# Kernel tuning notes

Hardware: AMD Instinct MI355X
Metric: run time of the kernel (lower is better)

Reference implementation:

```python
import jax, jax.numpy as jnp
import numpy as np

N = 8192          # total genes
B = 16            # number of ragged batch groups (equal-size here: 512 each)
D = 768           # hidden_dim
NEG = -1.0e9      # mask fill value used by the original module


def setup_inputs() -> dict:
    key = jax.random.key(0)
    ks = jax.random.split(key, 10)
    s = 0.02
    inp = {
        "gene_embeddings": jax.random.normal(ks[0], (N, D), dtype=jnp.float32),
        # sorted group ids: 16 contiguous groups of 512 genes
        "batch": (jnp.arange(N) // (N // B)).astype(jnp.int64),
        "Wq": jax.random.normal(ks[1], (D, D), dtype=jnp.float32) * s,
        "bq": jnp.zeros((D,), dtype=jnp.float32),
        "Wk": jax.random.normal(ks[2], (D, D), dtype=jnp.float32) * s,
        "bk": jnp.zeros((D,), dtype=jnp.float32),
        "Wv": jax.random.normal(ks[3], (D, D), dtype=jnp.float32) * s,
        "bv": jnp.zeros((D,), dtype=jnp.float32),
        "Wo": jax.random.normal(ks[4], (D, D), dtype=jnp.float32) * s,
        "bo": jnp.zeros((D,), dtype=jnp.float32),
        "beta": jnp.ones((1,), dtype=jnp.float32) * 0.1,
    }
    return inp


def reference(gene_embeddings, batch, Wq, bq, Wk, bk, Wv, bv, Wo, bo, beta):
    # Single-head attention over full hidden_dim (num_heads unused in original).
    x = gene_embeddings
    q = x @ Wq.T + bq                      # [N, D]
    k = x @ Wk.T + bk
    v = x @ Wv.T + bv
    scale = 1.0 / jnp.sqrt(jnp.asarray(D, dtype=x.dtype))
    scores = (q @ k.T) * scale             # [N, N]
    # block-diagonal group mask + diagonal self-mask (same -1e9 fill as torch code)
    same_group = batch[:, None] == batch[None, :]
    eye = jnp.eye(N, dtype=bool)
    allow = same_group & (~eye)
    scores = jnp.where(allow, scores, NEG)
    weights = jax.nn.softmax(scores, axis=-1)   # dropout in eval mode -> identity
    dyn = weights @ v                       # [N, D]
    dyn = dyn @ Wo.T + bo
    return x + beta * dyn
```

## Files before the change

kernel.cpp:

```cpp
#include <hip/hip_runtime.h>
#include <hip/hip_bf16.h>
#include <cstdint>

using u16 = unsigned short;
using u32 = unsigned int;

typedef __bf16 bf16x8 __attribute__((ext_vector_type(8)));
typedef float  f32x4  __attribute__((ext_vector_type(4)));

__device__ __forceinline__ u32 f2b2(float a, float b) {
    __hip_bfloat162 h = __float22bfloat162_rn(float2{a, b});
    u32 u;
    __builtin_memcpy(&u, &h, 4);
    return u;
}
__device__ __forceinline__ float b2f(u16 b) {
    u32 u = (u32)b << 16;
    float f;
    __builtin_memcpy(&f, &u, 4);
    return f;
}

__device__ __forceinline__ void gload_lds16(const u16* g, u16* l) {
    __builtin_amdgcn_global_load_lds(
        (const __attribute__((address_space(1))) void*)g,
        (__attribute__((address_space(3))) void*)l,
        16, 0, 0);
}

__launch_bounds__(256)
__global__ void pack_kernel(const float* __restrict__ x,
                            const float* __restrict__ Wq,
                            const float* __restrict__ Wk,
                            const float* __restrict__ Wv,
                            const float* __restrict__ Wo,
                            const float* __restrict__ bq,
                            const float* __restrict__ bv,
                            const float* __restrict__ bo,
                            u16* __restrict__ xb,
                            u16* __restrict__ Wob,
                            u16* __restrict__ WqT,
                            u16* __restrict__ WkT,
                            u16* __restrict__ WvT,
                            float* __restrict__ czk,
                            float* __restrict__ bvoo)
{
    __shared__ u16 tl[64][72];
    const int b = blockIdx.x, tid = threadIdx.x;

    if (b < 3360) {
        int c = b * 256 + tid;
        long e = (long)c * 8;
        const float* src; u16* dst; long off;
        if (e < 6291456L) { src = x;  dst = xb;  off = e; }
        else              { src = Wo; dst = Wob; off = e - 6291456L; }
        float4 v0 = *(const float4*)(src + off);
        float4 v1 = *(const float4*)(src + off + 4);
        uint4 o;
        o.x = f2b2(v0.x, v0.y); o.y = f2b2(v0.z, v0.w);
        o.z = f2b2(v1.x, v1.y); o.w = f2b2(v1.z, v1.w);
        *(uint4*)(dst + off) = o;
    } else if (b < 3792) {
        int t = b - 3360;
        int w = t / 144, tt = t % 144;
        int tr = tt / 12, tc = tt % 12;
        const float* src0 = (w == 0) ? Wq : (w == 1) ? Wk : Wv;
        u16* dst0 = (w == 0) ? WqT : (w == 1) ? WkT : WvT;
        int lr = tid >> 2, lcb = (tid & 3) * 16;
        const float* src = src0 + (long)(tr * 64 + lr) * 768 + tc * 64 + lcb;
#pragma unroll
        for (int q = 0; q < 4; q++) {
            float4 v = *(const float4*)(src + q * 4);
            u32 p0 = f2b2(v.x, v.y), p1 = f2b2(v.z, v.w);
            tl[lr][lcb + q * 4 + 0] = (u16)p0;
            tl[lr][lcb + q * 4 + 1] = (u16)(p0 >> 16);
            tl[lr][lcb + q * 4 + 2] = (u16)p1;
            tl[lr][lcb + q * 4 + 3] = (u16)(p1 >> 16);
        }
        __syncthreads();
        int li = tid >> 2, lkb = (tid & 3) * 16;
        u16 o[16];
#pragma unroll
        for (int j = 0; j < 16; j++) o[j] = tl[lkb + j][li];
        u16* dst = dst0 + (long)(tc * 64 + li) * 768 + tr * 64 + lkb;
#pragma unroll
        for (int j = 0; j < 16; j++) dst[j] = o[j];
    } else if (b < 3984) {
        int wave = tid >> 6, lane = tid & 63;
        int j = (b - 3792) * 4 + wave;
        float acc = 0.f;
#pragma unroll
        for (int i = 0; i < 12; i++) {
            int rr = i * 64 + lane;
            acc += Wk[(long)rr * 768 + j] * bq[rr];
        }
#pragma unroll
        for (int d = 32; d; d >>= 1) acc += __shfl_xor(acc, d);
        if (lane == 0) czk[j] = acc;
    } else {
        int wave = tid >> 6, lane = tid & 63;
        int j = (b - 3984) * 4 + wave;
        float acc = 0.f;
#pragma unroll
        for (int i = 0; i < 12; i++) {
            int k = i * 64 + lane;
            acc += Wo[(long)j * 768 + k] * bv[k];
        }
#pragma unroll
        for (int d = 32; d; d >>= 1) acc += __shfl_xor(acc, d);
        if (lane == 0) bvoo[j] = acc + bo[j];
    }
}

template<int TM, int TN, int MODE>
__device__ __forceinline__ void gemm_body(
        const u16* __restrict__ A, int lda, long sAz,
        const u16* __restrict__ B, int ldb, long sBz,
        void* __restrict__ Cv, int ldc, long sCz,
        int K,
        const float* __restrict__ bias,
        float scale,
        u16* __restrict__ vTout)
{
    constexpr int FI = TM / 32;
    constexpr int FJ = TN / 32;
    constexpr int CA = TM / 64;
    constexpr int CB = TN / 64;

    __shared__ u16 As[2][TM * 32];
    __shared__ u16 Bs[2][TN * 32];

    const int tid  = threadIdx.x;
    const int g    = blockIdx.z;
    const u16* Ab = A + (long)g * sAz + (long)blockIdx.y * TM * lda;
    const u16* Bb = B + (long)g * sBz + (long)blockIdx.x * TN * ldb;

    const int wave = tid >> 6, lane = tid & 63;
    const int wm = (wave >> 1) * (TM / 2), wn = (wave & 1) * (TN / 2);
    const int ln15 = lane & 15, lq = lane >> 4;

    f32x4 acc[FI][FJ];
#pragma unroll
    for (int i = 0; i < FI; i++)
#pragma unroll
        for (int j = 0; j < FJ; j++)
            acc[i][j] = (f32x4){0.f, 0.f, 0.f, 0.f};

    const int srow = lane >> 2;
    const int sc   = ((lane & 3) ^ ((lane >> 4) & 3)) * 8;
    const u16* Ag[CA]; const u16* Bg[CB];
    int Al[CA], Bl[CB];
#pragma unroll
    for (int t = 0; t < CA; t++) {
        int c = wave * CA + t;
        Ag[t] = Ab + (long)(c * 16 + srow) * lda + sc;
        Al[t] = c * 512;
    }
#pragma unroll
    for (int t = 0; t < CB; t++) {
        int c = wave * CB + t;
        Bg[t] = Bb + (long)(c * 16 + srow) * ldb + sc;
        Bl[t] = c * 512;
    }

    const int foff = ln15 * 32 + ((lq ^ (ln15 >> 2)) * 8);
    const int nk = K >> 5;

#pragma unroll
    for (int t = 0; t < CA; t++) gload_lds16(Ag[t], &As[0][Al[t]]);
#pragma unroll
    for (int t = 0; t < CB; t++) gload_lds16(Bg[t], &Bs[0][Bl[t]]);

    for (int kt = 0; kt < nk; kt++) {
        const int cur = kt & 1;
        __syncthreads();
        if (kt + 1 < nk) {
            const int k0 = (kt + 1) * 32, nxt = cur ^ 1;
#pragma unroll
            for (int t = 0; t < CA; t++) gload_lds16(Ag[t] + k0, &As[nxt][Al[t]]);
#pragma unroll
            for (int t = 0; t < CB; t++) gload_lds16(Bg[t] + k0, &Bs[nxt][Bl[t]]);
        }

        bf16x8 af[FI], bfr[FJ];
#pragma unroll
        for (int i = 0; i < FI; i++)
            af[i] = *(const bf16x8*)&As[cur][(wm / 16 + i) * 512 + foff];
#pragma unroll
        for (int j = 0; j < FJ; j++)
            bfr[j] = *(const bf16x8*)&Bs[cur][(wn / 16 + j) * 512 + foff];
#pragma unroll
        for (int i = 0; i < FI; i++)
#pragma unroll
            for (int j = 0; j < FJ; j++)
                acc[i][j] = __builtin_amdgcn_mfma_f32_16x16x32_bf16(af[i], bfr[j], acc[i][j], 0, 0, 0);
    }

    const int baseRow = blockIdx.y * TM + wm;
    const int baseCol = blockIdx.x * TN + wn;

    if constexpr (MODE == 0) {
        if (baseCol < 768) {
            u16* C = (u16*)Cv;
#pragma unroll
            for (int i = 0; i < FI; i++)
#pragma unroll
                for (int j = 0; j < FJ; j++) {
                    int col = baseCol + j * 16 + ln15;
                    float bb = bias[col];
                    u32 p01 = f2b2(acc[i][j][0] + bb, acc[i][j][1] + bb);
                    u32 p23 = f2b2(acc[i][j][2] + bb, acc[i][j][3] + bb);
                    long r0 = (long)(baseRow + i * 16 + lq * 4) * ldc + col;
                    C[r0]           = (u16)p01;
                    C[r0 + ldc]     = (u16)(p01 >> 16);
                    C[r0 + 2 * ldc] = (u16)p23;
                    C[r0 + 3 * ldc] = (u16)(p23 >> 16);
                }
        } else {
#pragma unroll
            for (int i = 0; i < FI; i++)
#pragma unroll
                for (int j = 0; j < FJ; j++) {
                    int col = baseCol + j * 16 + ln15;
                    uint2 o;
                    o.x = f2b2(acc[i][j][0], acc[i][j][1]);
                    o.y = f2b2(acc[i][j][2], acc[i][j][3]);
                    *(uint2*)(vTout + (long)(col - 768) * 8192
                              + baseRow + i * 16 + lq * 4) = o;
                }
        }
    } else {
        u16* C = (u16*)Cv + (long)g * sCz;
#pragma unroll
        for (int i = 0; i < FI; i++)
#pragma unroll
            for (int j = 0; j < FJ; j++) {
                int col = baseCol + j * 16 + ln15;
                u32 p01 = f2b2(acc[i][j][0], acc[i][j][1]);
                u32 p23 = f2b2(acc[i][j][2], acc[i][j][3]);
                long r0 = (long)(baseRow + i * 16 + lq * 4) * ldc + col;
                C[r0]           = (u16)p01;
                C[r0 + ldc]     = (u16)(p01 >> 16);
                C[r0 + 2 * ldc] = (u16)p23;
                C[r0 + 3 * ldc] = (u16)(p23 >> 16);
            }
    }
}

__launch_bounds__(256)
__global__ void k_ww(const u16* WA, const u16* WB, void* WZplus)
{
    gemm_body<64, 128, 3>(WA, 768, 589824L, WB, 768, 589824L,
                          WZplus, 768, -589824L, 768,
                          nullptr, 0.f, nullptr);
}
__launch_bounds__(256)
__global__ void k_zv(const u16* A, const u16* B, void* C, const float* bias,
                     u16* vTout)
{
    gemm_body<128, 128, 0>(A, 768, 0, B, 768, 0, C, 768, 0, 768,
                           bias, 0.f, vTout);
}

__launch_bounds__(512)
__global__ void k_fattn(const u16* __restrict__ zbuf,
                        const u16* __restrict__ xb,
                        const u16* __restrict__ vwT,
                        float* __restrict__ out,
                        const float* __restrict__ bvoo,
                        const float* __restrict__ betaPtr,
                        float scale)
{
    __shared__ __align__(16) u16 smem[57344];
    u16* zl = smem;
    u16* xB = smem + 24576;
    u16* Pl = smem;
    float* redM = (float*)(smem + 16384);
    float* redS = (float*)(smem + 16640);
    u16* Vs = smem + 18432;

    const int bx = blockIdx.x;
    const int lg = ((bx & 7) << 5) + (bx >> 3);
    const int g = lg >> 4, rt = lg & 15;

    const int tid = threadIdx.x;
    const int wave = tid >> 6, lane = tid & 63;
    const int ln15 = lane & 15, lq = lane >> 4;
    const int srow = lane >> 2;
    const int sc = ((lane & 3) ^ ((lane >> 4) & 3)) * 8;
    const int foff = ln15 * 32 + ((lq ^ (ln15 >> 2)) * 8);

    const long rowBase = (long)(g * 512 + rt * 32);
    const u16* Zb = zbuf + rowBase * 768;
    const u16* Xg = xb + (long)g * 512 * 768;

    const int wm = (wave >> 2) * 16;
    const int wn = (wave & 3) * 128;

#pragma unroll
    for (int n = 0; n < 6; n++) {
        int cc = n * 8 + wave;
        gload_lds16(Zb + (long)((cc & 1) * 16 + srow) * 768 + (cc >> 1) * 32 + sc,
                    &zl[cc * 512]);
    }
    const u16* Bg[4]; int Bl[4];
#pragma unroll
    for (int t = 0; t < 4; t++) {
        int c = wave * 4 + t;
        Bg[t] = Xg + (long)(c * 16 + srow) * 768 + sc;
        Bl[t] = c * 512;
    }
#pragma unroll
    for (int t = 0; t < 4; t++) gload_lds16(Bg[t], &xB[Bl[t]]);

    f32x4 acc[8];
#pragma unroll
    for (int j = 0; j < 8; j++) acc[j] = (f32x4){0.f, 0.f, 0.f, 0.f};

    for (int kt = 0; kt < 24; kt++) {
        const int cur = kt & 1;
        __syncthreads();
        if (kt + 1 < 24) {
            const int k0 = (kt + 1) * 32, nxt = cur ^ 1;
#pragma unroll
            for (int t = 0; t < 4; t++)
                gload_lds16(Bg[t] + k0, &xB[nxt * 16384 + Bl[t]]);
        }
        bf16x8 af = *(const bf16x8*)&zl[(kt * 2 + (wm >> 4)) * 512 + foff];
        bf16x8 bfr[8];
#pragma unroll
        for (int j = 0; j < 8; j++)
            bfr[j] = *(const bf16x8*)&xB[cur * 16384 + (wn / 16 + j) * 512 + foff];
#pragma unroll
        for (int j = 0; j < 8; j++)
            acc[j] = __builtin_amdgcn_mfma_f32_16x16x32_bf16(af, bfr[j], acc[j], 0, 0, 0);
    }

    __syncthreads();

#pragma unroll
    for (int sub = 0; sub < 4; sub++)
        gload_lds16(vwT + (long)(wave * 16 + srow) * 8192 + g * 512 + sub * 32 + sc,
                    &Vs[sub * 4096 + wave * 512]);

    float mx[4];
#pragma unroll
    for (int rr = 0; rr < 4; rr++) mx[rr] = -3.0e38f;
#pragma unroll
    for (int j = 0; j < 8; j++)
#pragma unroll
        for (int rr = 0; rr < 4; rr++) {
            const int col = wn + j * 16 + ln15;
            float v = acc[j][rr] * scale;
            if (rt * 32 + wm + lq * 4 + rr == col) v = -1.0e9f;
            acc[j][rr] = v;
            mx[rr] = fmaxf(mx[rr], v);
        }
#pragma unroll
    for (int rr = 0; rr < 4; rr++) {
        mx[rr] = fmaxf(mx[rr], __shfl_xor(mx[rr], 1));
        mx[rr] = fmaxf(mx[rr], __shfl_xor(mx[rr], 2));
        mx[rr] = fmaxf(mx[rr], __shfl_xor(mx[rr], 4));
        mx[rr] = fmaxf(mx[rr], __shfl_xor(mx[rr], 8));
    }
    if (ln15 == 0) {
#pragma unroll
        for (int rr = 0; rr < 4; rr++)
            redM[(wm + lq * 4 + rr) * 4 + (wave & 3)] = mx[rr];
    }
    __syncthreads();

    float m[4], s[4];
#pragma unroll
    for (int rr = 0; rr < 4; rr++) {
        float4 rm = *(const float4*)&redM[(wm + lq * 4 + rr) * 4];
        m[rr] = fmaxf(fmaxf(rm.x, rm.y), fmaxf(rm.z, rm.w));
        s[rr] = 0.f;
    }
#pragma unroll
    for (int j = 0; j < 8; j++)
#pragma unroll
        for (int rr = 0; rr < 4; rr++) {
            float p = __expf(acc[j][rr] - m[rr]);
            acc[j][rr] = p;
            s[rr] += p;
        }
#pragma unroll
    for (int rr = 0; rr < 4; rr++) {
        s[rr] += __shfl_xor(s[rr], 1);
        s[rr] += __shfl_xor(s[rr], 2);
        s[rr] += __shfl_xor(s[rr], 4);
        s[rr] += __shfl_xor(s[rr], 8);
    }
    if (ln15 == 0) {
#pragma unroll
        for (int rr = 0; rr < 4; rr++)
            redS[(wm + lq * 4 + rr) * 4 + (wave & 3)] = s[rr];
    }
#pragma unroll
    for (int j = 0; j < 8; j++) {
        const int col = wn + j * 16 + ln15;
        const int c8 = col >> 3, b7 = col & 7;
#pragma unroll
        for (int rr = 0; rr < 4; rr++) {
            const int row = wm + lq * 4 + rr;
            Pl[(row * 64 + (c8 ^ (row & 7))) * 8 + b7] = (u16)f2b2(acc[j][rr], acc[j][rr]);
        }
    }
    __syncthreads();

    float invS[4];
#pragma unroll
    for (int rr = 0; rr < 4; rr++) {
        float4 rs = *(const float4*)&redS[(wm + lq * 4 + rr) * 4];
        invS[rr] = 1.0f / (rs.x + rs.y + rs.z + rs.w);
    }

    const int prow = wm + ln15;
    bf16x8 apr[16];
#pragma unroll
    for (int k4 = 0; k4 < 16; k4++)
        apr[k4] = *(const bf16x8*)&Pl[(prow * 64 + ((k4 * 4 + lq) ^ (prow & 7))) * 8];

    const int wnP = (wave & 3) * 32;
    const float bet = betaPtr[0];
    f32x4 aP0 = (f32x4){0.f, 0.f, 0.f, 0.f};
    f32x4 aP1 = (f32x4){0.f, 0.f, 0.f, 0.f};

    for (int ct = 0; ct < 6; ct++) {
#pragma unroll
        for (int kn2 = 0; kn2 < 4; kn2++) {
            const int ts = ct * 4 + kn2;
            const int cur = ts & 1;
            __syncthreads();
            if (ts + 1 < 24) {
                const int tn = ts + 1, ctn = tn >> 2, kn = tn & 3;
                const int nxt = cur ^ 1;
#pragma unroll
                for (int sub = 0; sub < 4; sub++)
                    gload_lds16(vwT + (long)(ctn * 128 + wave * 16 + srow) * 8192
                                    + g * 512 + kn * 128 + sub * 32 + sc,
                                &Vs[nxt * 16384 + sub * 4096 + wave * 512]);
            }
#pragma unroll
            for (int sub = 0; sub < 4; sub++) {
                bf16x8 b0 = *(const bf16x8*)&Vs[cur * 16384 + sub * 4096
                                                + (wnP >> 4) * 512 + foff];
                bf16x8 b1 = *(const bf16x8*)&Vs[cur * 16384 + sub * 4096
                                                + ((wnP >> 4) + 1) * 512 + foff];
                aP0 = __builtin_amdgcn_mfma_f32_16x16x32_bf16(apr[kn2 * 4 + sub], b0, aP0, 0, 0, 0);
                aP1 = __builtin_amdgcn_mfma_f32_16x16x32_bf16(apr[kn2 * 4 + sub], b1, aP1, 0, 0, 0);
            }
        }
        {
            const u16* Xr = xb + (rowBase + wm + lq * 4) * 768;
            float* O = out + (rowBase + wm + lq * 4) * 768;
            {
                const int col = ct * 128 + wnP + ln15;
                const float bb = bvoo[col];
#pragma unroll
                for (int rr = 0; rr < 4; rr++)
                    O[rr * 768 + col] = b2f(Xr[rr * 768 + col])
                                        + bet * (invS[rr] * aP0[rr] + bb);
            }
            {
                const int col = ct * 128 + wnP + 16 + ln15;
                const float bb = bvoo[col];
#pragma unroll
                for (int rr = 0; rr < 4; rr++)
                    O[rr * 768 + col] = b2f(Xr[rr * 768 + col])
                                        + bet * (invS[rr] * aP1[rr] + bb);
            }
            aP0 = (f32x4){0.f, 0.f, 0.f, 0.f};
            aP1 = (f32x4){0.f, 0.f, 0.f, 0.f};
        }
    }
}

extern "C" void kernel_launch(void* const* d_in, const int* in_sizes, int n_in,
                              void* d_out, int out_size, void* d_ws, size_t ws_size,
                              hipStream_t stream)
{
    const float* x    = (const float*)d_in[0];
    const float* Wq   = (const float*)d_in[2];
    const float* bq   = (const float*)d_in[3];
    const float* Wk   = (const float*)d_in[4];
    const float* bk   = (const float*)d_in[5];
    const float* Wv   = (const float*)d_in[6];
    const float* bv   = (const float*)d_in[7];
    const float* Wo   = (const float*)d_in[8];
    const float* bo   = (const float*)d_in[9];
    const float* beta = (const float*)d_in[10];
    float* out = (float*)d_out;
    (void)bk;

    char* ws = (char*)d_ws;
    u16*   zbuf = (u16*)(ws + 0);
    u16*   vwT  = (u16*)(ws + 12582912);
    u16*   xb   = (u16*)(ws + 25165824);
    u16*   WA   = (u16*)(ws + 46137344);
    u16*   WB   = (u16*)(ws + 48496640);
    u16*   WZ   = (u16*)(ws + 50855936);
    float* czk  = (float*)(ws + 53215232);
    float* bvoo = (float*)(ws + 53218304);

    u16* Wob = WA;
    u16* WkT = WA + 589824;
    u16* WvT = WB;
    u16* WqT = WB + 589824;

    const float scale = 0.03608439182435161f;

    pack_kernel<<<4176, 256, 0, stream>>>(x, Wq, Wk, Wv, Wo, bq, bv, bo,
                                          xb, Wob, WqT, WkT, WvT, czk, bvoo);

    k_ww<<<dim3(6, 12, 2), 256, 0, stream>>>(WA, WB, (void*)(WZ + 589824L));

    k_zv<<<dim3(12, 64, 1), 256, 0, stream>>>(xb, WZ, (void*)zbuf, czk, vwT);

    k_fattn<<<dim3(256), 512, 0, stream>>>(zbuf, xb, vwT, out, bvoo, beta,
                                           scale);
}
```

Baseline: 193.9 us.

## Deepen LDS prefetch to two stages with explicit waitcnt and deferred epilogue

The QK^T and PV loops now issue global-to-LDS loads two tiles ahead instead of one. __syncthreads is replaced by explicit vmcnt/lgkmcnt waits and raw barriers, and s_setprio is raised around the MFMA bursts. In the PV stage, all six column-tile accumulators are kept in registers and the output epilogue is moved after the loop, so global loads and stores no longer sit between MFMA phases. The aim is to hide load latency and barrier stalls, at the cost of more registers, a second barrier per iteration, and hand-written wait counts that have to match the number of loads in flight.

```diff
diff --git a/kernel.cpp b/kernel.cpp
--- a/kernel.cpp
+++ b/kernel.cpp
@@ -27,6 +27,10 @@
         (__attribute__((address_space(3))) void*)l,
         16, 0, 0);
 }
+
+#define VMCNT(N)  asm volatile("s_waitcnt vmcnt(" #N ")" ::: "memory")
+#define LGKMCNT0  asm volatile("s_waitcnt lgkmcnt(0)" ::: "memory")
+#define BARRIER   asm volatile("s_barrier" ::: "memory")
 
 __launch_bounds__(256)
 __global__ void pack_kernel(const float* __restrict__ x,
@@ -312,6 +316,8 @@
     }
 #pragma unroll
     for (int t = 0; t < 4; t++) gload_lds16(Bg[t], &xB[Bl[t]]);
+#pragma unroll
+    for (int t = 0; t < 4; t++) gload_lds16(Bg[t] + 32, &xB[16384 + Bl[t]]);
 
     f32x4 acc[8];
 #pragma unroll
@@ -319,21 +325,27 @@
 
     for (int kt = 0; kt < 24; kt++) {
         const int cur = kt & 1;
-        __syncthreads();
-        if (kt + 1 < 24) {
-            const int k0 = (kt + 1) * 32, nxt = cur ^ 1;
-#pragma unroll
-            for (int t = 0; t < 4; t++)
-                gload_lds16(Bg[t] + k0, &xB[nxt * 16384 + Bl[t]]);
-        }
+        if (kt < 23) { VMCNT(4); } else { VMCNT(0); }
+        BARRIER;
         bf16x8 af = *(const bf16x8*)&zl[(kt * 2 + (wm >> 4)) * 512 + foff];
         bf16x8 bfr[8];
 #pragma unroll
         for (int j = 0; j < 8; j++)
             bfr[j] = *(const bf16x8*)&xB[cur * 16384 + (wn / 16 + j) * 512 + foff];
+        LGKMCNT0;
+        __builtin_amdgcn_sched_barrier(0);
+        BARRIER;
+        if (kt + 2 < 24) {
+            const int k0 = (kt + 2) * 32;
+#pragma unroll
+            for (int t = 0; t < 4; t++)
+                gload_lds16(Bg[t] + k0, &xB[cur * 16384 + Bl[t]]);
+        }
+        __builtin_amdgcn_s_setprio(1);
 #pragma unroll
         for (int j = 0; j < 8; j++)
             acc[j] = __builtin_amdgcn_mfma_f32_16x16x32_bf16(af, bfr[j], acc[j], 0, 0, 0);
+        __builtin_amdgcn_s_setprio(0);
     }
 
     __syncthreads();
@@ -342,6 +354,10 @@
     for (int sub = 0; sub < 4; sub++)
         gload_lds16(vwT + (long)(wave * 16 + srow) * 8192 + g * 512 + sub * 32 + sc,
                     &Vs[sub * 4096 + wave * 512]);
+#pragma unroll
+    for (int sub = 0; sub < 4; sub++)
+        gload_lds16(vwT + (long)(wave * 16 + srow) * 8192 + g * 512 + 128 + sub * 32 + sc,
+                    &Vs[16384 + sub * 4096 + wave * 512]);
 
     float mx[4];
 #pragma unroll
@@ -423,56 +439,63 @@
         apr[k4] = *(const bf16x8*)&Pl[(prow * 64 + ((k4 * 4 + lq) ^ (prow & 7))) * 8];
 
     const int wnP = (wave & 3) * 32;
-    const float bet = betaPtr[0];
-    f32x4 aP0 = (f32x4){0.f, 0.f, 0.f, 0.f};
-    f32x4 aP1 = (f32x4){0.f, 0.f, 0.f, 0.f};
-
+    f32x4 aP[6][2];
+#pragma unroll
+    for (int ct = 0; ct < 6; ct++) {
+        aP[ct][0] = (f32x4){0.f, 0.f, 0.f, 0.f};
+        aP[ct][1] = (f32x4){0.f, 0.f, 0.f, 0.f};
+    }
+
+#pragma unroll
     for (int ct = 0; ct < 6; ct++) {
 #pragma unroll
         for (int kn2 = 0; kn2 < 4; kn2++) {
             const int ts = ct * 4 + kn2;
             const int cur = ts & 1;
-            __syncthreads();
-            if (ts + 1 < 24) {
-                const int tn = ts + 1, ctn = tn >> 2, kn = tn & 3;
-                const int nxt = cur ^ 1;
+            if (ts < 23) { VMCNT(4); } else { VMCNT(0); }
+            BARRIER;
+            bf16x8 b0[4], b1[4];
+#pragma unroll
+            for (int sub = 0; sub < 4; sub++) {
+                b0[sub] = *(const bf16x8*)&Vs[cur * 16384 + sub * 4096
+                                              + (wnP >> 4) * 512 + foff];
+                b1[sub] = *(const bf16x8*)&Vs[cur * 16384 + sub * 4096
+                                              + ((wnP >> 4) + 1) * 512 + foff];
+            }
+            LGKMCNT0;
+            __builtin_amdgcn_sched_barrier(0);
+            BARRIER;
+            if (ts + 2 < 24) {
+                const int tn = ts + 2, ctn = tn >> 2, kn = tn & 3;
 #pragma unroll
                 for (int sub = 0; sub < 4; sub++)
                     gload_lds16(vwT + (long)(ctn * 128 + wave * 16 + srow) * 8192
                                     + g * 512 + kn * 128 + sub * 32 + sc,
-                                &Vs[nxt * 16384 + sub * 4096 + wave * 512]);
+                                &Vs[cur * 16384 + sub * 4096 + wave * 512]);
             }
+            __builtin_amdgcn_s_setprio(1);
 #pragma unroll
             for (int sub = 0; sub < 4; sub++) {
-                bf16x8 b0 = *(const bf16x8*)&Vs[cur * 16384 + sub * 4096
-                                                + (wnP >> 4) * 512 + foff];
-                bf16x8 b1 = *(const bf16x8*)&Vs[cur * 16384 + sub * 4096
-                                                + ((wnP >> 4) + 1) * 512 + foff];
-                aP0 = __builtin_amdgcn_mfma_f32_16x16x32_bf16(apr[kn2 * 4 + sub], b0, aP0, 0, 0, 0);
-                aP1 = __builtin_amdgcn_mfma_f32_16x16x32_bf16(apr[kn2 * 4 + sub], b1, aP1, 0, 0, 0);
+                aP[ct][0] = __builtin_amdgcn_mfma_f32_16x16x32_bf16(apr[kn2 * 4 + sub], b0[sub], aP[ct][0], 0, 0, 0);
+                aP[ct][1] = __builtin_amdgcn_mfma_f32_16x16x32_bf16(apr[kn2 * 4 + sub], b1[sub], aP[ct][1], 0, 0, 0);
             }
-        }
-        {
-            const u16* Xr = xb + (rowBase + wm + lq * 4) * 768;
-            float* O = out + (rowBase + wm + lq * 4) * 768;
-            {
-                const int col = ct * 128 + wnP + ln15;
-                const float bb = bvoo[col];
-#pragma unroll
-                for (int rr = 0; rr < 4; rr++)
-                    O[rr * 768 + col] = b2f(Xr[rr * 768 + col])
-                                        + bet * (invS[rr] * aP0[rr] + bb);
-            }
-            {
-                const int col = ct * 128 + wnP + 16 + ln15;
-                const float bb = bvoo[col];
-#pragma unroll
-                for (int rr = 0; rr < 4; rr++)
-                    O[rr * 768 + col] = b2f(Xr[rr * 768 + col])
-                                        + bet * (invS[rr] * aP1[rr] + bb);
-            }
-            aP0 = (f32x4){0.f, 0.f, 0.f, 0.f};
-            aP1 = (f32x4){0.f, 0.f, 0.f, 0.f};
+            __builtin_amdgcn_s_setprio(0);
+        }
+    }
+
+    const float bet = betaPtr[0];
+    const u16* Xr = xb + (rowBase + wm + lq * 4) * 768;
+    float* O = out + (rowBase + wm + lq * 4) * 768;
+#pragma unroll
+    for (int ct = 0; ct < 6; ct++) {
+#pragma unroll
+        for (int jj = 0; jj < 2; jj++) {
+            const int col = ct * 128 + wnP + jj * 16 + ln15;
+            const float bb = bvoo[col];
+#pragma unroll
+            for (int rr = 0; rr < 4; rr++)
+                O[rr * 768 + col] = b2f(Xr[rr * 768 + col])
+                                    + bet * (invS[rr] * aP[ct][jj][rr] + bb);
         }
     }
 }
```

After: 191.8 us. Within noise of the previous version (-1.1%).
